# Optimization experiments

Hardware: AMD Instinct MI355X
Metric: run time of the kernel (lower is better)

Reference implementation:

```python
import jax, jax.numpy as jnp
import numpy as np

ROUNDS = 2
N_NODES = 50000
N_EDGES = 800000
NODE_DIM = 128
EDGE_DIM = 32
ACT_DIM = 128


def setup_inputs() -> dict:
    key = jax.random.key(0)
    ks = jax.random.split(key, 10)
    hv = jax.random.normal(ks[0], (N_NODES, NODE_DIM), dtype=jnp.float32)
    he = jax.random.normal(ks[1], (N_EDGES, EDGE_DIM), dtype=jnp.float32)
    src = jax.random.randint(ks[2], (N_EDGES,), 0, N_NODES, dtype=jnp.int32)
    dst = jax.random.randint(ks[3], (N_EDGES,), 0, N_NODES, dtype=jnp.int32)
    cat_dim = 2 * NODE_DIM + EDGE_DIM  # 288
    W_msg = jax.random.normal(ks[4], (ROUNDS, cat_dim, ACT_DIM), dtype=jnp.float32) * 0.05
    b_msg = jax.random.normal(ks[5], (ROUNDS, ACT_DIM), dtype=jnp.float32) * 0.05
    W_ih = jax.random.normal(ks[6], (ROUNDS, ACT_DIM, 3 * NODE_DIM), dtype=jnp.float32) * 0.05
    W_hh = jax.random.normal(ks[7], (ROUNDS, NODE_DIM, 3 * NODE_DIM), dtype=jnp.float32) * 0.05
    b_ih = jax.random.normal(ks[8], (ROUNDS, 3 * NODE_DIM), dtype=jnp.float32) * 0.05
    b_hh = jax.random.normal(ks[9], (ROUNDS, 3 * NODE_DIM), dtype=jnp.float32) * 0.05
    return {"hv": hv, "he": he, "src": src, "dst": dst,
            "W_msg": W_msg, "b_msg": b_msg,
            "W_ih": W_ih, "W_hh": W_hh, "b_ih": b_ih, "b_hh": b_hh}


def _gru_cell(x, h, W_ih, W_hh, b_ih, b_hh):
    # torch.nn.GRUCell math, gate order (r, z, n)
    gi = x @ W_ih + b_ih  # [N, 3H]
    gh = h @ W_hh + b_hh  # [N, 3H]
    ir, iz, in_ = jnp.split(gi, 3, axis=-1)
    hr, hz, hn = jnp.split(gh, 3, axis=-1)
    r = jax.nn.sigmoid(ir + hr)
    z = jax.nn.sigmoid(iz + hz)
    n = jnp.tanh(in_ + r * hn)
    return (1.0 - z) * n + z * h


def reference(hv, he, src, dst, W_msg, b_msg, W_ih, W_hh, b_ih, b_hh):
    N, nd = hv.shape
    for t in range(ROUNDS):
        # Linear on concat([hv_src, hv_dst, he]) == sum of block matmuls
        Ws = W_msg[t, :nd]          # src block
        Wd = W_msg[t, nd:2 * nd]    # dst block
        We = W_msg[t, 2 * nd:]      # edge block
        msg = hv[src] @ Ws + hv[dst] @ Wd + he @ We + b_msg[t]  # [E, act]
        a = jax.ops.segment_sum(msg, dst, num_segments=N)        # per-node sum over incoming edges
        hv = _gru_cell(a, hv, W_ih[t], W_hh[t], b_ih[t], b_hh[t])
    return hv
```

## Files before the change

kernel.cpp:

```cpp
#include <hip/hip_runtime.h>

#define N_NODES 50000
#define N_EDGES 800000
#define ND 128
#define ED 32
#define AD 128
#define CAT 288
#define G3 384

#define XPAD 296
#define KSTEPS 9
#define SCAN_BS 512

typedef unsigned short ushort_t;
typedef __attribute__((ext_vector_type(8))) short bfrag;
typedef __attribute__((ext_vector_type(4))) float f32x4;

__device__ __forceinline__ unsigned int f2bf(float f) {
    unsigned int u = __float_as_uint(f);
    return (u + 0x7FFFu + ((u >> 16) & 1u)) >> 16;
}
__device__ __forceinline__ void split2(float a, float b,
                                       unsigned int& hi, unsigned int& lo) {
    const unsigned int ha = f2bf(a), hb = f2bf(b);
    const float ra = a - __uint_as_float(ha << 16);
    const float rb = b - __uint_as_float(hb << 16);
    hi = ha | (hb << 16);
    lo = f2bf(ra) | (f2bf(rb) << 16);
}
__device__ __forceinline__ void split1(float a, ushort_t& hi, ushort_t& lo) {
    const unsigned int ha = f2bf(a);
    const float ra = a - __uint_as_float(ha << 16);
    hi = (ushort_t)ha;
    lo = (ushort_t)f2bf(ra);
}

__global__ __launch_bounds__(256) void hist_kernel(
    const int* __restrict__ dst, int* __restrict__ deg)
{
    const int e = blockIdx.x * 256 + threadIdx.x;
    if (e < N_EDGES) atomicAdd(&deg[dst[e]], 1);
}

__global__ __launch_bounds__(SCAN_BS) void scan_block_kernel(
    const int* __restrict__ in, int* __restrict__ out,
    int* __restrict__ bsum, int n)
{
    __shared__ int s[SCAN_BS];
    const int g = blockIdx.x * SCAN_BS + threadIdx.x;
    const int v = (g < n) ? in[g] : 0;
    s[threadIdx.x] = v;
    __syncthreads();
    for (int off = 1; off < SCAN_BS; off <<= 1) {
        const int x = (threadIdx.x >= off) ? s[threadIdx.x - off] : 0;
        __syncthreads();
        s[threadIdx.x] += x;
        __syncthreads();
    }
    if (g < n) out[g] = s[threadIdx.x] - v;
    if (threadIdx.x == SCAN_BS - 1) bsum[blockIdx.x] = s[threadIdx.x];
}

__global__ __launch_bounds__(128) void scan_sums_kernel(int* __restrict__ bsum, int nb)
{
    __shared__ int s[128];
    const int i = threadIdx.x;
    s[i] = (i < nb) ? bsum[i] : 0;
    __syncthreads();
    if (i == 0) {
        int acc = 0;
        for (int k = 0; k < nb; ++k) { const int t = s[k]; s[k] = acc; acc += t; }
    }
    __syncthreads();
    if (i < nb) bsum[i] = s[i];
}

__global__ __launch_bounds__(SCAN_BS) void scan_add_kernel(
    int* __restrict__ rowptr, int* __restrict__ cursor,
    const int* __restrict__ bsum, int n)
{
    const int g = blockIdx.x * SCAN_BS + threadIdx.x;
    if (g < n) {
        const int v = rowptr[g] + bsum[blockIdx.x];
        rowptr[g] = v;
        cursor[g] = v;
    }
}

__global__ __launch_bounds__(256) void fill_kernel(
    const int* __restrict__ dst, const int* __restrict__ src,
    int* __restrict__ cursor, int* __restrict__ perm,
    int* __restrict__ src_sorted)
{
    const int e = blockIdx.x * 256 + threadIdx.x;
    if (e < N_EDGES) {
        const int p = atomicAdd(&cursor[dst[e]], 1);
        perm[p] = e;
        src_sorted[p] = src[e];
    }
}

__global__ __launch_bounds__(256) void esum_kernel(
    const float* __restrict__ he, const int* __restrict__ perm,
    const int* __restrict__ rowptr, float* __restrict__ E)
{
    const int id = blockIdx.x * 256 + threadIdx.x;
    if (id >= N_NODES * ED) return;
    const int v = id >> 5, c = id & 31;
    const int r0 = rowptr[v], r1 = rowptr[v + 1];
    float s = 0.f;
    int i = r0;
    for (; i + 4 <= r1; i += 4) {
        const int p0 = perm[i],     p1 = perm[i + 1];
        const int p2 = perm[i + 2], p3 = perm[i + 3];
        const float a = he[(size_t)p0 * ED + c];
        const float b = he[(size_t)p1 * ED + c];
        const float d = he[(size_t)p2 * ED + c];
        const float f = he[(size_t)p3 * ED + c];
        s += (a + b) + (d + f);
    }
    for (; i < r1; ++i)
        s += he[(size_t)perm[i] * ED + c];
    E[(size_t)v * ED + c] = s;
}

__global__ __launch_bounds__(256) void convert_w_kernel(
    const float* __restrict__ W,
    ushort_t* __restrict__ Wt_hi, ushort_t* __restrict__ Wt_lo)
{
    const int id = blockIdx.x * 256 + threadIdx.x;
    if (id >= 2 * CAT * AD) return;
    const int n = id & (AD - 1);
    const int k = (id >> 7) % CAT;
    const int t = id / (CAT * AD);
    const float w = W[(size_t)t * CAT * AD + (size_t)k * AD + n];
    const unsigned int hi = f2bf(w);
    const float r = w - __uint_as_float(hi << 16);
    const size_t o = (size_t)t * AD * CAT + (size_t)n * CAT + k;
    Wt_hi[o] = (ushort_t)hi;
    Wt_lo[o] = (ushort_t)f2bf(r);
}

__global__ __launch_bounds__(256) void convert_gatew_kernel(
    const float* __restrict__ W_ih, const float* __restrict__ W_hh,
    ushort_t* __restrict__ Bih_hi, ushort_t* __restrict__ Bih_lo,
    ushort_t* __restrict__ Bhh_hi, ushort_t* __restrict__ Bhh_lo)
{
    const int id = blockIdx.x * 256 + threadIdx.x;
    if (id >= 196608) return;
    const int t   = id / 98304;
    const int rem = id % 98304;
    const int mat = rem / 49152;
    const int q   = rem % 49152;
    const int nt = q / 2048,  r1 = q % 2048;
    const int ks = r1 / 512,  r2 = r1 % 512;
    const int kq = r2 / 128,  r3 = r2 % 128;
    const int lr = r3 / 8,    j  = r3 % 8;
    const int n = nt * 16 + lr;
    const int k = ks * 32 + kq * 8 + j;
    const float* W = mat ? W_hh : W_ih;
    const float w = W[(size_t)t * ND * G3 + (size_t)k * G3 + n];
    const unsigned int hi = f2bf(w);
    const float res = w - __uint_as_float(hi << 16);
    const size_t o = (size_t)t * 49152 + q;
    if (mat) { Bhh_hi[o] = (ushort_t)hi; Bhh_lo[o] = (ushort_t)f2bf(res); }
    else     { Bih_hi[o] = (ushort_t)hi; Bih_lo[o] = (ushort_t)f2bf(res); }
}

__global__ __launch_bounds__(256) void agg_kernel(
    const float* __restrict__ hv, const int* __restrict__ src_sorted,
    const int* __restrict__ rowptr,
    ushort_t* __restrict__ S_hi, ushort_t* __restrict__ S_lo)
{
    const int v = blockIdx.x * 4 + (threadIdx.x >> 6);
    if (v >= N_NODES) return;
    const int lane = threadIdx.x & 63;
    const int r0 = rowptr[v], r1 = rowptr[v + 1];
    const float2* hv2 = (const float2*)hv;
    float sx = 0.f, sy = 0.f;
    int i = r0;
    for (; i + 8 <= r1; i += 8) {
        const int s0 = src_sorted[i],     s1 = src_sorted[i + 1];
        const int s2 = src_sorted[i + 2], s3 = src_sorted[i + 3];
        const int s4 = src_sorted[i + 4], s5 = src_sorted[i + 5];
        const int s6 = src_sorted[i + 6], s7 = src_sorted[i + 7];
        const float2 a = hv2[(size_t)s0 * 64 + lane];
        const float2 b = hv2[(size_t)s1 * 64 + lane];
        const float2 c = hv2[(size_t)s2 * 64 + lane];
        const float2 d = hv2[(size_t)s3 * 64 + lane];
        const float2 e = hv2[(size_t)s4 * 64 + lane];
        const float2 f = hv2[(size_t)s5 * 64 + lane];
        const float2 g = hv2[(size_t)s6 * 64 + lane];
        const float2 h = hv2[(size_t)s7 * 64 + lane];
        sx += ((a.x + b.x) + (c.x + d.x)) + ((e.x + f.x) + (g.x + h.x));
        sy += ((a.y + b.y) + (c.y + d.y)) + ((e.y + f.y) + (g.y + h.y));
    }
    for (; i < r1; ++i) {
        const float2 a = hv2[(size_t)src_sorted[i] * 64 + lane];
        sx += a.x; sy += a.y;
    }
    unsigned int h, l;
    split2(sx, sy, h, l);
    ((unsigned int*)S_hi)[(size_t)v * 64 + lane] = h;
    ((unsigned int*)S_lo)[(size_t)v * 64 + lane] = l;
}

__global__ __launch_bounds__(256, 2) void fused_msg_gru_kernel(
    const ushort_t* __restrict__ S_hi, const ushort_t* __restrict__ S_lo,
    const float* __restrict__ h_cur, const float* __restrict__ E,
    const int* __restrict__ rowptr,
    const ushort_t* __restrict__ Wt_hi, const ushort_t* __restrict__ Wt_lo,
    const float* __restrict__ bmsg,
    const ushort_t* __restrict__ Bih_hi, const ushort_t* __restrict__ Bih_lo,
    const ushort_t* __restrict__ Bhh_hi, const ushort_t* __restrict__ Bhh_lo,
    const float* __restrict__ b_ih, const float* __restrict__ b_hh,
    float* __restrict__ h_out)
{
    __shared__ __align__(16) char smem[67072];
    ushort_t* xh    = (ushort_t*)smem;
    ushort_t* xl    = xh + 32 * XPAD;
    ushort_t* sh_hi = xl + 32 * XPAD;
    ushort_t* sh_lo = sh_hi + 32 * 136;
    ushort_t* sa_hi = (ushort_t*)smem;
    ushort_t* sa_lo = sa_hi + 32 * 136;
    float* grz = (float*)smem;
    float* gin = grz + 32 * 260;
    float* ghn = gin + 32 * 132;
    __shared__ float sdeg[32];

    const int t    = threadIdx.x;
    const int wave = t >> 6;
    const int lane = t & 63;
    const int kq   = lane >> 4;
    const int lr   = lane & 15;
    const int n0   = blockIdx.x * 32;

    bfrag mbh[2][KSTEPS], mbl[2][KSTEPS];
    float mbias[2];
    #pragma unroll
    for (int nt = 0; nt < 2; ++nt) {
        const int n = wave * 32 + nt * 16 + lr;
        mbias[nt] = bmsg[n];
        const ushort_t* ph = Wt_hi + (size_t)n * CAT + kq * 8;
        const ushort_t* pl = Wt_lo + (size_t)n * CAT + kq * 8;
        #pragma unroll
        for (int ks = 0; ks < KSTEPS; ++ks) {
            mbh[nt][ks] = *(const bfrag*)(ph + ks * 32);
            mbl[nt][ks] = *(const bfrag*)(pl + ks * 32);
        }
    }

    {
        const int row = t >> 3, c8 = t & 7;
        const int n = min(n0 + row, N_NODES - 1);
        if (t < 32) {
            const int nn = min(n0 + t, N_NODES - 1);
            sdeg[t] = (float)(rowptr[nn + 1] - rowptr[nn]);
        }
        {
            const uint4* ph = (const uint4*)(S_hi + (size_t)n * ND + c8 * 16);
            const uint4* pl = (const uint4*)(S_lo + (size_t)n * ND + c8 * 16);
            *(uint4*)&xh[row * XPAD + c8 * 16]     = ph[0];
            *(uint4*)&xh[row * XPAD + c8 * 16 + 8] = ph[1];
            *(uint4*)&xl[row * XPAD + c8 * 16]     = pl[0];
            *(uint4*)&xl[row * XPAD + c8 * 16 + 8] = pl[1];
        }
        {
            const float degf = (float)(rowptr[n + 1] - rowptr[n]);
            const float4* hp = (const float4*)(h_cur + (size_t)n * ND + c8 * 16);
            const float4 v0 = hp[0], v1 = hp[1], v2 = hp[2], v3 = hp[3];
            uint4 h0, h1, l0, l1;
            split2(v0.x, v0.y, h0.x, l0.x); split2(v0.z, v0.w, h0.y, l0.y);
            split2(v1.x, v1.y, h0.z, l0.z); split2(v1.z, v1.w, h0.w, l0.w);
            split2(v2.x, v2.y, h1.x, l1.x); split2(v2.z, v2.w, h1.y, l1.y);
            split2(v3.x, v3.y, h1.z, l1.z); split2(v3.z, v3.w, h1.w, l1.w);
            const int so = row * 136 + c8 * 16;
            *(uint4*)(sh_hi + so) = h0;  *(uint4*)(sh_hi + so + 8) = h1;
            *(uint4*)(sh_lo + so) = l0;  *(uint4*)(sh_lo + so + 8) = l1;
            uint4 g0, g1, m0, m1;
            split2(v0.x * degf, v0.y * degf, g0.x, m0.x); split2(v0.z * degf, v0.w * degf, g0.y, m0.y);
            split2(v1.x * degf, v1.y * degf, g0.z, m0.z); split2(v1.z * degf, v1.w * degf, g0.w, m0.w);
            split2(v2.x * degf, v2.y * degf, g1.x, m1.x); split2(v2.z * degf, v2.w * degf, g1.y, m1.y);
            split2(v3.x * degf, v3.y * degf, g1.z, m1.z); split2(v3.z * degf, v3.w * degf, g1.w, m1.w);
            *(uint4*)&xh[row * XPAD + ND + c8 * 16]     = g0;
            *(uint4*)&xh[row * XPAD + ND + c8 * 16 + 8] = g1;
            *(uint4*)&xl[row * XPAD + ND + c8 * 16]     = m0;
            *(uint4*)&xl[row * XPAD + ND + c8 * 16 + 8] = m1;
        }
        {
            const float4 e4 = *(const float4*)(E + (size_t)n * ED + c8 * 4);
            uint2 h0, l0;
            split2(e4.x, e4.y, h0.x, l0.x); split2(e4.z, e4.w, h0.y, l0.y);
            *(uint2*)&xh[row * XPAD + 2 * ND + c8 * 4] = h0;
            *(uint2*)&xl[row * XPAD + 2 * ND + c8 * 4] = l0;
        }
    }
    __syncthreads();

    f32x4 acc00 = {0.f,0.f,0.f,0.f}, acc01 = {0.f,0.f,0.f,0.f};
    f32x4 acc10 = {0.f,0.f,0.f,0.f}, acc11 = {0.f,0.f,0.f,0.f};
    #pragma unroll
    for (int ks = 0; ks < KSTEPS; ++ks) {
        const int ko = ks * 32 + kq * 8;
        const bfrag a0h = *(const bfrag*)&xh[lr * XPAD + ko];
        const bfrag a0l = *(const bfrag*)&xl[lr * XPAD + ko];
        const bfrag a1h = *(const bfrag*)&xh[(16 + lr) * XPAD + ko];
        const bfrag a1l = *(const bfrag*)&xl[(16 + lr) * XPAD + ko];
        acc00 = __builtin_amdgcn_mfma_f32_16x16x32_bf16(a0h, mbh[0][ks], acc00, 0, 0, 0);
        acc00 = __builtin_amdgcn_mfma_f32_16x16x32_bf16(a0l, mbh[0][ks], acc00, 0, 0, 0);
        acc00 = __builtin_amdgcn_mfma_f32_16x16x32_bf16(a0h, mbl[0][ks], acc00, 0, 0, 0);
        acc01 = __builtin_amdgcn_mfma_f32_16x16x32_bf16(a0h, mbh[1][ks], acc01, 0, 0, 0);
        acc01 = __builtin_amdgcn_mfma_f32_16x16x32_bf16(a0l, mbh[1][ks], acc01, 0, 0, 0);
        acc01 = __builtin_amdgcn_mfma_f32_16x16x32_bf16(a0h, mbl[1][ks], acc01, 0, 0, 0);
        acc10 = __builtin_amdgcn_mfma_f32_16x16x32_bf16(a1h, mbh[0][ks], acc10, 0, 0, 0);
        acc10 = __builtin_amdgcn_mfma_f32_16x16x32_bf16(a1l, mbh[0][ks], acc10, 0, 0, 0);
        acc10 = __builtin_amdgcn_mfma_f32_16x16x32_bf16(a1h, mbl[0][ks], acc10, 0, 0, 0);
        acc11 = __builtin_amdgcn_mfma_f32_16x16x32_bf16(a1h, mbh[1][ks], acc11, 0, 0, 0);
        acc11 = __builtin_amdgcn_mfma_f32_16x16x32_bf16(a1l, mbh[1][ks], acc11, 0, 0, 0);
        acc11 = __builtin_amdgcn_mfma_f32_16x16x32_bf16(a1h, mbl[1][ks], acc11, 0, 0, 0);
    }
    __syncthreads();

    #pragma unroll
    for (int r = 0; r < 4; ++r) {
        const int row0 = kq * 4 + r;
        const int row1 = 16 + kq * 4 + r;
        const int c0 = wave * 32 + lr, c1 = wave * 32 + 16 + lr;
        ushort_t h, l;
        split1(acc00[r] + sdeg[row0] * mbias[0], h, l);
        sa_hi[row0 * 136 + c0] = h; sa_lo[row0 * 136 + c0] = l;
        split1(acc01[r] + sdeg[row0] * mbias[1], h, l);
        sa_hi[row0 * 136 + c1] = h; sa_lo[row0 * 136 + c1] = l;
        split1(acc10[r] + sdeg[row1] * mbias[0], h, l);
        sa_hi[row1 * 136 + c0] = h; sa_lo[row1 * 136 + c0] = l;
        split1(acc11[r] + sdeg[row1] * mbias[1], h, l);
        sa_hi[row1 * 136 + c1] = h; sa_lo[row1 * 136 + c1] = l;
    }
    __syncthreads();

    f32x4 acc_i[2][6], acc_h[2][6];
    #pragma unroll
    for (int m = 0; m < 2; ++m)
        #pragma unroll
        for (int nt = 0; nt < 6; ++nt) {
            acc_i[m][nt] = (f32x4){0.f, 0.f, 0.f, 0.f};
            acc_h[m][nt] = (f32x4){0.f, 0.f, 0.f, 0.f};
        }

    #pragma unroll
    for (int ks = 0; ks < 4; ++ks) {
        bfrag afh[2], afl[2], hfh[2], hfl[2];
        #pragma unroll
        for (int m = 0; m < 2; ++m) {
            const int ao = (m * 16 + lr) * 136 + ks * 32 + kq * 8;
            afh[m] = *(const bfrag*)(sa_hi + ao);
            afl[m] = *(const bfrag*)(sa_lo + ao);
            hfh[m] = *(const bfrag*)(sh_hi + ao);
            hfl[m] = *(const bfrag*)(sh_lo + ao);
        }
        #pragma unroll
        for (int nt = 0; nt < 6; ++nt) {
            const int gnt = wave * 6 + nt;
            const int bo = (((gnt * 4 + ks) * 4 + kq) * 16 + lr) * 8;
            const bfrag bih_h = *(const bfrag*)(Bih_hi + bo);
            const bfrag bih_l = *(const bfrag*)(Bih_lo + bo);
            const bfrag bhh_h = *(const bfrag*)(Bhh_hi + bo);
            const bfrag bhh_l = *(const bfrag*)(Bhh_lo + bo);
            #pragma unroll
            for (int m = 0; m < 2; ++m) {
                acc_i[m][nt] = __builtin_amdgcn_mfma_f32_16x16x32_bf16(afh[m], bih_h, acc_i[m][nt], 0, 0, 0);
                acc_i[m][nt] = __builtin_amdgcn_mfma_f32_16x16x32_bf16(afl[m], bih_h, acc_i[m][nt], 0, 0, 0);
                acc_i[m][nt] = __builtin_amdgcn_mfma_f32_16x16x32_bf16(afh[m], bih_l, acc_i[m][nt], 0, 0, 0);
                acc_h[m][nt] = __builtin_amdgcn_mfma_f32_16x16x32_bf16(hfh[m], bhh_h, acc_h[m][nt], 0, 0, 0);
                acc_h[m][nt] = __builtin_amdgcn_mfma_f32_16x16x32_bf16(hfl[m], bhh_h, acc_h[m][nt], 0, 0, 0);
                acc_h[m][nt] = __builtin_amdgcn_mfma_f32_16x16x32_bf16(hfh[m], bhh_l, acc_h[m][nt], 0, 0, 0);
            }
        }
    }
    __syncthreads();

    #pragma unroll
    for (int nt = 0; nt < 6; ++nt) {
        const int gcol = wave * 96 + nt * 16 + lr;
        if (gcol < 256) {
            const float bias = b_ih[gcol] + b_hh[gcol];
            #pragma unroll
            for (int m = 0; m < 2; ++m)
                #pragma unroll
                for (int r = 0; r < 4; ++r)
                    grz[(m * 16 + kq * 4 + r) * 260 + gcol] =
                        acc_i[m][nt][r] + acc_h[m][nt][r] + bias;
        } else {
            const int cc = gcol - 256;
            const float bi = b_ih[gcol], bh2 = b_hh[gcol];
            #pragma unroll
            for (int m = 0; m < 2; ++m)
                #pragma unroll
                for (int r = 0; r < 4; ++r) {
                    const int rw = m * 16 + kq * 4 + r;
                    gin[rw * 132 + cc] = acc_i[m][nt][r] + bi;
                    ghn[rw * 132 + cc] = acc_h[m][nt][r] + bh2;
                }
        }
    }
    __syncthreads();

    for (int idx = t; idx < 32 * ND; idx += 256) {
        const int nl = idx >> 7, cc = idx & 127;
        const int n = n0 + nl;
        if (n < N_NODES) {
            const float rp  = grz[nl * 260 + cc];
            const float zp  = grz[nl * 260 + 128 + cc];
            const float inp = gin[nl * 132 + cc];
            const float hnp = ghn[nl * 132 + cc];
            const float r = 1.f / (1.f + expf(-rp));
            const float z = 1.f / (1.f + expf(-zp));
            const float nn = tanhf(inp + r * hnp);
            h_out[(size_t)n * ND + cc] =
                (1.f - z) * nn + z * h_cur[(size_t)n * ND + cc];
        }
    }
}

extern "C" void kernel_launch(void* const* d_in, const int* in_sizes, int n_in,
                              void* d_out, int out_size, void* d_ws, size_t ws_size,
                              hipStream_t stream)
{
    const float* hv   = (const float*)d_in[0];
    const float* he   = (const float*)d_in[1];
    const int*   src  = (const int*)d_in[2];
    const int*   dst  = (const int*)d_in[3];
    const float* Wmsg = (const float*)d_in[4];
    const float* bmsg = (const float*)d_in[5];
    const float* Wih  = (const float*)d_in[6];
    const float* Whh  = (const float*)d_in[7];
    const float* bih  = (const float*)d_in[8];
    const float* bhh  = (const float*)d_in[9];
    float* out = (float*)d_out;

    const int nscan = ((N_NODES + SCAN_BS - 1) / SCAN_BS) * SCAN_BS;
    const int nblk  = nscan / SCAN_BS;

    char* p = (char*)d_ws;
    ushort_t* S_hi = (ushort_t*)p;            p += (size_t)N_NODES * ND * 2;
    ushort_t* S_lo = (ushort_t*)p;            p += (size_t)N_NODES * ND * 2;
    float* E = (float*)p;                     p += (size_t)N_NODES * ED * 4;
    ushort_t* Wt_hi = (ushort_t*)p;           p += (size_t)2 * AD * CAT * 2;
    ushort_t* Wt_lo = (ushort_t*)p;           p += (size_t)2 * AD * CAT * 2;
    ushort_t* Bih_hi = (ushort_t*)p;          p += (size_t)2 * G3 * ND * 2;
    ushort_t* Bih_lo = (ushort_t*)p;          p += (size_t)2 * G3 * ND * 2;
    ushort_t* Bhh_hi = (ushort_t*)p;          p += (size_t)2 * G3 * ND * 2;
    ushort_t* Bhh_lo = (ushort_t*)p;          p += (size_t)2 * G3 * ND * 2;
    int* deg    = (int*)p;                    p += (size_t)nscan * 4;
    int* rowptr = (int*)p;                    p += (size_t)nscan * 4;
    int* cursor = (int*)p;                    p += (size_t)nscan * 4;
    int* bsum   = (int*)p;                    p += 128 * 4;
    int* perm   = (int*)p;                    p += (size_t)N_EDGES * 4;
    int* src_sorted = (int*)p;                p += (size_t)N_EDGES * 4;

    convert_w_kernel<<<(2 * CAT * AD + 255) / 256, 256, 0, stream>>>(Wmsg, Wt_hi, Wt_lo);
    convert_gatew_kernel<<<768, 256, 0, stream>>>(Wih, Whh, Bih_hi, Bih_lo, Bhh_hi, Bhh_lo);

    hipMemsetAsync(deg, 0, (size_t)nscan * 4, stream);
    hist_kernel<<<(N_EDGES + 255) / 256, 256, 0, stream>>>(dst, deg);
    scan_block_kernel<<<nblk, SCAN_BS, 0, stream>>>(deg, rowptr, bsum, nscan);
    scan_sums_kernel<<<1, 128, 0, stream>>>(bsum, nblk);
    scan_add_kernel<<<nblk, SCAN_BS, 0, stream>>>(rowptr, cursor, bsum, nscan);
    fill_kernel<<<(N_EDGES + 255) / 256, 256, 0, stream>>>(dst, src, cursor, perm, src_sorted);
    esum_kernel<<<(N_NODES * ED + 255) / 256, 256, 0, stream>>>(he, perm, rowptr, E);

    const int tile_blocks = (N_NODES + 31) / 32;

    for (int t = 0; t < 2; ++t) {
        const float* h_cur = (t == 0) ? hv : out;
        agg_kernel<<<(N_NODES + 3) / 4, 256, 0, stream>>>(
            h_cur, src_sorted, rowptr, S_hi, S_lo);
        fused_msg_gru_kernel<<<tile_blocks, 256, 0, stream>>>(
            S_hi, S_lo, h_cur, E, rowptr,
            Wt_hi + (size_t)t * AD * CAT, Wt_lo + (size_t)t * AD * CAT,
            bmsg + (size_t)t * AD,
            Bih_hi + (size_t)t * G3 * ND, Bih_lo + (size_t)t * G3 * ND,
            Bhh_hi + (size_t)t * G3 * ND, Bhh_lo + (size_t)t * G3 * ND,
            bih + (size_t)t * G3, bhh + (size_t)t * G3, out);
    }
}
```

Baseline: 583.4 us.

## Reuse h tile for dst-message term, stream weights, fuse GRU epilogue in registers

The degree-scaled h copy in the message GEMM's K dimension is dropped. The kernel now reuses the existing swizzled h tile, computing the dst term as a separate accumulator that is multiplied by degree afterwards. Message weights are streamed from global memory in MFMA fragment order instead of being held in registers. Gate weights are permuted so each wave owns matching r/z/n columns, which lets the GRU nonlinearity run directly on accumulators with fast exp instead of going through shared-memory staging. Shared memory and register use shrink so three blocks can fit per CU, at the cost of more global weight loads and fast-math approximations of sigmoid and tanh.

```diff
diff --git a/kernel.cpp b/kernel.cpp
--- a/kernel.cpp
+++ b/kernel.cpp
@@ -8,8 +8,7 @@
 #define CAT 288
 #define G3 384
 
-#define XPAD 296
-#define KSTEPS 9
+#define XP2 168
 #define SCAN_BS 512
 
 typedef unsigned short ushort_t;
@@ -130,13 +129,20 @@
 {
     const int id = blockIdx.x * 256 + threadIdx.x;
     if (id >= 2 * CAT * AD) return;
-    const int n = id & (AD - 1);
-    const int k = (id >> 7) % CAT;
-    const int t = id / (CAT * AD);
-    const float w = W[(size_t)t * CAT * AD + (size_t)k * AD + n];
+    const int tt = id / (CAT * AD);
+    const int q  = id % (CAT * AD);
+    const int j  = q & 7;
+    const int lr = (q >> 3) & 15;
+    const int kq = (q >> 7) & 3;
+    const int ks = (q >> 9) % 9;
+    const int gnt = q / 4608;
+    const int n  = gnt * 16 + lr;
+    const int kn = ks * 32 + kq * 8 + j;
+    const int ko = kn < 128 ? kn : (kn < 160 ? kn + 128 : kn - 32);
+    const float w = W[(size_t)tt * CAT * AD + (size_t)ko * AD + n];
     const unsigned int hi = f2bf(w);
     const float r = w - __uint_as_float(hi << 16);
-    const size_t o = (size_t)t * AD * CAT + (size_t)n * CAT + k;
+    const size_t o = (size_t)tt * (CAT * AD) + q;
     Wt_hi[o] = (ushort_t)hi;
     Wt_lo[o] = (ushort_t)f2bf(r);
 }
@@ -156,7 +162,9 @@
     const int ks = r1 / 512,  r2 = r1 % 512;
     const int kq = r2 / 128,  r3 = r2 % 128;
     const int lr = r3 / 8,    j  = r3 % 8;
-    const int n = nt * 16 + lr;
+    const int wv = nt / 6, within = nt % 6;
+    const int gate = within % 3, hf = within / 3;
+    const int n = gate * 128 + wv * 32 + hf * 16 + lr;
     const int k = ks * 32 + kq * 8 + j;
     const float* W = mat ? W_hh : W_ih;
     const float w = W[(size_t)t * ND * G3 + (size_t)k * G3 + n];
@@ -205,7 +213,7 @@
     ((unsigned int*)S_lo)[(size_t)v * 64 + lane] = l;
 }
 
-__global__ __launch_bounds__(256, 2) void fused_msg_gru_kernel(
+__global__ __launch_bounds__(256, 3) void fused_msg_gru_kernel(
     const ushort_t* __restrict__ S_hi, const ushort_t* __restrict__ S_lo,
     const float* __restrict__ h_cur, const float* __restrict__ E,
     const int* __restrict__ rowptr,
@@ -216,16 +224,13 @@
     const float* __restrict__ b_ih, const float* __restrict__ b_hh,
     float* __restrict__ h_out)
 {
-    __shared__ __align__(16) char smem[67072];
+    __shared__ __align__(16) char smem[37888];
     ushort_t* xh    = (ushort_t*)smem;
-    ushort_t* xl    = xh + 32 * XPAD;
-    ushort_t* sh_hi = xl + 32 * XPAD;
-    ushort_t* sh_lo = sh_hi + 32 * 136;
+    ushort_t* xl    = xh + 32 * XP2;
+    ushort_t* sh_hi = xl + 32 * XP2;
+    ushort_t* sh_lo = sh_hi + 32 * 128;
     ushort_t* sa_hi = (ushort_t*)smem;
-    ushort_t* sa_lo = sa_hi + 32 * 136;
-    float* grz = (float*)smem;
-    float* gin = grz + 32 * 260;
-    float* ghn = gin + 32 * 132;
+    ushort_t* sa_lo = sa_hi + 32 * 128;
     __shared__ float sdeg[32];
 
     const int t    = threadIdx.x;
@@ -235,20 +240,8 @@
     const int lr   = lane & 15;
     const int n0   = blockIdx.x * 32;
 
-    bfrag mbh[2][KSTEPS], mbl[2][KSTEPS];
-    float mbias[2];
-    #pragma unroll
-    for (int nt = 0; nt < 2; ++nt) {
-        const int n = wave * 32 + nt * 16 + lr;
-        mbias[nt] = bmsg[n];
-        const ushort_t* ph = Wt_hi + (size_t)n * CAT + kq * 8;
-        const ushort_t* pl = Wt_lo + (size_t)n * CAT + kq * 8;
-        #pragma unroll
-        for (int ks = 0; ks < KSTEPS; ++ks) {
-            mbh[nt][ks] = *(const bfrag*)(ph + ks * 32);
-            mbl[nt][ks] = *(const bfrag*)(pl + ks * 32);
-        }
-    }
+    const float mbias0 = bmsg[wave * 32 + lr];
+    const float mbias1 = bmsg[wave * 32 + 16 + lr];
 
     {
         const int row = t >> 3, c8 = t & 7;
@@ -260,13 +253,12 @@
         {
             const uint4* ph = (const uint4*)(S_hi + (size_t)n * ND + c8 * 16);
             const uint4* pl = (const uint4*)(S_lo + (size_t)n * ND + c8 * 16);
-            *(uint4*)&xh[row * XPAD + c8 * 16]     = ph[0];
-            *(uint4*)&xh[row * XPAD + c8 * 16 + 8] = ph[1];
-            *(uint4*)&xl[row * XPAD + c8 * 16]     = pl[0];
-            *(uint4*)&xl[row * XPAD + c8 * 16 + 8] = pl[1];
+            *(uint4*)&xh[row * XP2 + c8 * 16]     = ph[0];
+            *(uint4*)&xh[row * XP2 + c8 * 16 + 8] = ph[1];
+            *(uint4*)&xl[row * XP2 + c8 * 16]     = pl[0];
+            *(uint4*)&xl[row * XP2 + c8 * 16 + 8] = pl[1];
         }
         {
-            const float degf = (float)(rowptr[n + 1] - rowptr[n]);
             const float4* hp = (const float4*)(h_cur + (size_t)n * ND + c8 * 16);
             const float4 v0 = hp[0], v1 = hp[1], v2 = hp[2], v3 = hp[3];
             uint4 h0, h1, l0, l1;
@@ -274,151 +266,160 @@
             split2(v1.x, v1.y, h0.z, l0.z); split2(v1.z, v1.w, h0.w, l0.w);
             split2(v2.x, v2.y, h1.x, l1.x); split2(v2.z, v2.w, h1.y, l1.y);
             split2(v3.x, v3.y, h1.z, l1.z); split2(v3.z, v3.w, h1.w, l1.w);
-            const int so = row * 136 + c8 * 16;
-            *(uint4*)(sh_hi + so) = h0;  *(uint4*)(sh_hi + so + 8) = h1;
-            *(uint4*)(sh_lo + so) = l0;  *(uint4*)(sh_lo + so + 8) = l1;
-            uint4 g0, g1, m0, m1;
-            split2(v0.x * degf, v0.y * degf, g0.x, m0.x); split2(v0.z * degf, v0.w * degf, g0.y, m0.y);
-            split2(v1.x * degf, v1.y * degf, g0.z, m0.z); split2(v1.z * degf, v1.w * degf, g0.w, m0.w);
-            split2(v2.x * degf, v2.y * degf, g1.x, m1.x); split2(v2.z * degf, v2.w * degf, g1.y, m1.y);
-            split2(v3.x * degf, v3.y * degf, g1.z, m1.z); split2(v3.z * degf, v3.w * degf, g1.w, m1.w);
-            *(uint4*)&xh[row * XPAD + ND + c8 * 16]     = g0;
-            *(uint4*)&xh[row * XPAD + ND + c8 * 16 + 8] = g1;
-            *(uint4*)&xl[row * XPAD + ND + c8 * 16]     = m0;
-            *(uint4*)&xl[row * XPAD + ND + c8 * 16 + 8] = m1;
+            const int so  = (row * 128 + c8 * 16)     ^ ((row & 7) << 3);
+            const int so2 = (row * 128 + c8 * 16 + 8) ^ ((row & 7) << 3);
+            *(uint4*)(sh_hi + so)  = h0;  *(uint4*)(sh_hi + so2) = h1;
+            *(uint4*)(sh_lo + so)  = l0;  *(uint4*)(sh_lo + so2) = l1;
         }
         {
             const float4 e4 = *(const float4*)(E + (size_t)n * ED + c8 * 4);
             uint2 h0, l0;
             split2(e4.x, e4.y, h0.x, l0.x); split2(e4.z, e4.w, h0.y, l0.y);
-            *(uint2*)&xh[row * XPAD + 2 * ND + c8 * 4] = h0;
-            *(uint2*)&xl[row * XPAD + 2 * ND + c8 * 4] = l0;
-        }
-    }
-    __syncthreads();
-
-    f32x4 acc00 = {0.f,0.f,0.f,0.f}, acc01 = {0.f,0.f,0.f,0.f};
-    f32x4 acc10 = {0.f,0.f,0.f,0.f}, acc11 = {0.f,0.f,0.f,0.f};
-    #pragma unroll
-    for (int ks = 0; ks < KSTEPS; ++ks) {
-        const int ko = ks * 32 + kq * 8;
-        const bfrag a0h = *(const bfrag*)&xh[lr * XPAD + ko];
-        const bfrag a0l = *(const bfrag*)&xl[lr * XPAD + ko];
-        const bfrag a1h = *(const bfrag*)&xh[(16 + lr) * XPAD + ko];
-        const bfrag a1l = *(const bfrag*)&xl[(16 + lr) * XPAD + ko];
-        acc00 = __builtin_amdgcn_mfma_f32_16x16x32_bf16(a0h, mbh[0][ks], acc00, 0, 0, 0);
-        acc00 = __builtin_amdgcn_mfma_f32_16x16x32_bf16(a0l, mbh[0][ks], acc00, 0, 0, 0);
-        acc00 = __builtin_amdgcn_mfma_f32_16x16x32_bf16(a0h, mbl[0][ks], acc00, 0, 0, 0);
-        acc01 = __builtin_amdgcn_mfma_f32_16x16x32_bf16(a0h, mbh[1][ks], acc01, 0, 0, 0);
-        acc01 = __builtin_amdgcn_mfma_f32_16x16x32_bf16(a0l, mbh[1][ks], acc01, 0, 0, 0);
-        acc01 = __builtin_amdgcn_mfma_f32_16x16x32_bf16(a0h, mbl[1][ks], acc01, 0, 0, 0);
-        acc10 = __builtin_amdgcn_mfma_f32_16x16x32_bf16(a1h, mbh[0][ks], acc10, 0, 0, 0);
-        acc10 = __builtin_amdgcn_mfma_f32_16x16x32_bf16(a1l, mbh[0][ks], acc10, 0, 0, 0);
-        acc10 = __builtin_amdgcn_mfma_f32_16x16x32_bf16(a1h, mbl[0][ks], acc10, 0, 0, 0);
-        acc11 = __builtin_amdgcn_mfma_f32_16x16x32_bf16(a1h, mbh[1][ks], acc11, 0, 0, 0);
-        acc11 = __builtin_amdgcn_mfma_f32_16x16x32_bf16(a1l, mbh[1][ks], acc11, 0, 0, 0);
-        acc11 = __builtin_amdgcn_mfma_f32_16x16x32_bf16(a1h, mbl[1][ks], acc11, 0, 0, 0);
+            *(uint2*)&xh[row * XP2 + 128 + c8 * 4] = h0;
+            *(uint2*)&xl[row * XP2 + 128 + c8 * 4] = l0;
+        }
+    }
+    __syncthreads();
+
+    f32x4 aX00 = {0.f,0.f,0.f,0.f}, aX01 = {0.f,0.f,0.f,0.f};
+    f32x4 aX10 = {0.f,0.f,0.f,0.f}, aX11 = {0.f,0.f,0.f,0.f};
+    f32x4 aP00 = {0.f,0.f,0.f,0.f}, aP01 = {0.f,0.f,0.f,0.f};
+    f32x4 aP10 = {0.f,0.f,0.f,0.f}, aP11 = {0.f,0.f,0.f,0.f};
+    {
+        const size_t wb0 = (size_t)(wave * 2 + 0) * 4608 + kq * 128 + lr * 8;
+        const size_t wb1 = (size_t)(wave * 2 + 1) * 4608 + kq * 128 + lr * 8;
+        const ushort_t* wh0 = Wt_hi + wb0;  const ushort_t* wl0 = Wt_lo + wb0;
+        const ushort_t* wh1 = Wt_hi + wb1;  const ushort_t* wl1 = Wt_lo + wb1;
+        #pragma unroll
+        for (int ks = 0; ks < 5; ++ks) {
+            const int ko = ks * 32 + kq * 8;
+            const bfrag a0h = *(const bfrag*)&xh[lr * XP2 + ko];
+            const bfrag a0l = *(const bfrag*)&xl[lr * XP2 + ko];
+            const bfrag a1h = *(const bfrag*)&xh[(16 + lr) * XP2 + ko];
+            const bfrag a1l = *(const bfrag*)&xl[(16 + lr) * XP2 + ko];
+            const bfrag b0h = *(const bfrag*)(wh0 + ks * 512);
+            const bfrag b0l = *(const bfrag*)(wl0 + ks * 512);
+            const bfrag b1h = *(const bfrag*)(wh1 + ks * 512);
+            const bfrag b1l = *(const bfrag*)(wl1 + ks * 512);
+            aX00 = __builtin_amdgcn_mfma_f32_16x16x32_bf16(a0h, b0h, aX00, 0, 0, 0);
+            aX00 = __builtin_amdgcn_mfma_f32_16x16x32_bf16(a0l, b0h, aX00, 0, 0, 0);
+            aX00 = __builtin_amdgcn_mfma_f32_16x16x32_bf16(a0h, b0l, aX00, 0, 0, 0);
+            aX01 = __builtin_amdgcn_mfma_f32_16x16x32_bf16(a0h, b1h, aX01, 0, 0, 0);
+            aX01 = __builtin_amdgcn_mfma_f32_16x16x32_bf16(a0l, b1h, aX01, 0, 0, 0);
+            aX01 = __builtin_amdgcn_mfma_f32_16x16x32_bf16(a0h, b1l, aX01, 0, 0, 0);
+            aX10 = __builtin_amdgcn_mfma_f32_16x16x32_bf16(a1h, b0h, aX10, 0, 0, 0);
+            aX10 = __builtin_amdgcn_mfma_f32_16x16x32_bf16(a1l, b0h, aX10, 0, 0, 0);
+            aX10 = __builtin_amdgcn_mfma_f32_16x16x32_bf16(a1h, b0l, aX10, 0, 0, 0);
+            aX11 = __builtin_amdgcn_mfma_f32_16x16x32_bf16(a1h, b1h, aX11, 0, 0, 0);
+            aX11 = __builtin_amdgcn_mfma_f32_16x16x32_bf16(a1l, b1h, aX11, 0, 0, 0);
+            aX11 = __builtin_amdgcn_mfma_f32_16x16x32_bf16(a1h, b1l, aX11, 0, 0, 0);
+        }
+        #pragma unroll
+        for (int ks = 5; ks < 9; ++ks) {
+            const int hk = (ks - 5) * 32 + kq * 8;
+            const int o0 = (lr * 128 + hk)        ^ ((lr & 7) << 3);
+            const int o1 = ((16 + lr) * 128 + hk) ^ ((lr & 7) << 3);
+            const bfrag a0h = *(const bfrag*)(sh_hi + o0);
+            const bfrag a0l = *(const bfrag*)(sh_lo + o0);
+            const bfrag a1h = *(const bfrag*)(sh_hi + o1);
+            const bfrag a1l = *(const bfrag*)(sh_lo + o1);
+            const bfrag b0h = *(const bfrag*)(wh0 + ks * 512);
+            const bfrag b0l = *(const bfrag*)(wl0 + ks * 512);
+            const bfrag b1h = *(const bfrag*)(wh1 + ks * 512);
+            const bfrag b1l = *(const bfrag*)(wl1 + ks * 512);
+            aP00 = __builtin_amdgcn_mfma_f32_16x16x32_bf16(a0h, b0h, aP00, 0, 0, 0);
+            aP00 = __builtin_amdgcn_mfma_f32_16x16x32_bf16(a0l, b0h, aP00, 0, 0, 0);
+            aP00 = __builtin_amdgcn_mfma_f32_16x16x32_bf16(a0h, b0l, aP00, 0, 0, 0);
+            aP01 = __builtin_amdgcn_mfma_f32_16x16x32_bf16(a0h, b1h, aP01, 0, 0, 0);
+            aP01 = __builtin_amdgcn_mfma_f32_16x16x32_bf16(a0l, b1h, aP01, 0, 0, 0);
+            aP01 = __builtin_amdgcn_mfma_f32_16x16x32_bf16(a0h, b1l, aP01, 0, 0, 0);
+            aP10 = __builtin_amdgcn_mfma_f32_16x16x32_bf16(a1h, b0h, aP10, 0, 0, 0);
+            aP10 = __builtin_amdgcn_mfma_f32_16x16x32_bf16(a1l, b0h, aP10, 0, 0, 0);
+            aP10 = __builtin_amdgcn_mfma_f32_16x16x32_bf16(a1h, b0l, aP10, 0, 0, 0);
+            aP11 = __builtin_amdgcn_mfma_f32_16x16x32_bf16(a1h, b1h, aP11, 0, 0, 0);
+            aP11 = __builtin_amdgcn_mfma_f32_16x16x32_bf16(a1l, b1h, aP11, 0, 0, 0);
+            aP11 = __builtin_amdgcn_mfma_f32_16x16x32_bf16(a1h, b1l, aP11, 0, 0, 0);
+        }
     }
     __syncthreads();
 
     #pragma unroll
     for (int r = 0; r < 4; ++r) {
         const int row0 = kq * 4 + r;
-        const int row1 = 16 + kq * 4 + r;
-        const int c0 = wave * 32 + lr, c1 = wave * 32 + 16 + lr;
+        const int row1 = 16 + row0;
+        const int c0 = wave * 32 + lr, c1 = c0 + 16;
+        const float d0 = sdeg[row0], d1 = sdeg[row1];
         ushort_t h, l;
-        split1(acc00[r] + sdeg[row0] * mbias[0], h, l);
-        sa_hi[row0 * 136 + c0] = h; sa_lo[row0 * 136 + c0] = l;
-        split1(acc01[r] + sdeg[row0] * mbias[1], h, l);
-        sa_hi[row0 * 136 + c1] = h; sa_lo[row0 * 136 + c1] = l;
-        split1(acc10[r] + sdeg[row1] * mbias[0], h, l);
-        sa_hi[row1 * 136 + c0] = h; sa_lo[row1 * 136 + c0] = l;
-        split1(acc11[r] + sdeg[row1] * mbias[1], h, l);
-        sa_hi[row1 * 136 + c1] = h; sa_lo[row1 * 136 + c1] = l;
-    }
-    __syncthreads();
-
-    f32x4 acc_i[2][6], acc_h[2][6];
+        split1(aX00[r] + d0 * (aP00[r] + mbias0), h, l);
+        { const int o = (row0 * 128 + c0) ^ ((row0 & 7) << 3); sa_hi[o] = h; sa_lo[o] = l; }
+        split1(aX01[r] + d0 * (aP01[r] + mbias1), h, l);
+        { const int o = (row0 * 128 + c1) ^ ((row0 & 7) << 3); sa_hi[o] = h; sa_lo[o] = l; }
+        split1(aX10[r] + d1 * (aP10[r] + mbias0), h, l);
+        { const int o = (row1 * 128 + c0) ^ ((row1 & 7) << 3); sa_hi[o] = h; sa_lo[o] = l; }
+        split1(aX11[r] + d1 * (aP11[r] + mbias1), h, l);
+        { const int o = (row1 * 128 + c1) ^ ((row1 & 7) << 3); sa_hi[o] = h; sa_lo[o] = l; }
+    }
+    __syncthreads();
+
     #pragma unroll
-    for (int m = 0; m < 2; ++m)
+    for (int half = 0; half < 2; ++half) {
+        f32x4 ai[2][3], ah2[2][3];
         #pragma unroll
-        for (int nt = 0; nt < 6; ++nt) {
-            acc_i[m][nt] = (f32x4){0.f, 0.f, 0.f, 0.f};
-            acc_h[m][nt] = (f32x4){0.f, 0.f, 0.f, 0.f};
-        }
-
-    #pragma unroll
-    for (int ks = 0; ks < 4; ++ks) {
-        bfrag afh[2], afl[2], hfh[2], hfl[2];
+        for (int m = 0; m < 2; ++m)
+            #pragma unroll
+            for (int g = 0; g < 3; ++g) {
+                ai[m][g]  = (f32x4){0.f, 0.f, 0.f, 0.f};
+                ah2[m][g] = (f32x4){0.f, 0.f, 0.f, 0.f};
+            }
         #pragma unroll
-        for (int m = 0; m < 2; ++m) {
-            const int ao = (m * 16 + lr) * 136 + ks * 32 + kq * 8;
-            afh[m] = *(const bfrag*)(sa_hi + ao);
-            afl[m] = *(const bfrag*)(sa_lo + ao);
-            hfh[m] = *(const bfrag*)(sh_hi + ao);
-            hfl[m] = *(const bfrag*)(sh_lo + ao);
-        }
-        #pragma unroll
-        for (int nt = 0; nt < 6; ++nt) {
-            const int gnt = wave * 6 + nt;
-            const int bo = (((gnt * 4 + ks) * 4 + kq) * 16 + lr) * 8;
-            const bfrag bih_h = *(const bfrag*)(Bih_hi + bo);
-            const bfrag bih_l = *(const bfrag*)(Bih_lo + bo);
-            const bfrag bhh_h = *(const bfrag*)(Bhh_hi + bo);
-            const bfrag bhh_l = *(const bfrag*)(Bhh_lo + bo);
+        for (int ks = 0; ks < 4; ++ks) {
+            bfrag afh[2], afl[2], hfh[2], hfl[2];
             #pragma unroll
             for (int m = 0; m < 2; ++m) {
-                acc_i[m][nt] = __builtin_amdgcn_mfma_f32_16x16x32_bf16(afh[m], bih_h, acc_i[m][nt], 0, 0, 0);
-                acc_i[m][nt] = __builtin_amdgcn_mfma_f32_16x16x32_bf16(afl[m], bih_h, acc_i[m][nt], 0, 0, 0);
-                acc_i[m][nt] = __builtin_amdgcn_mfma_f32_16x16x32_bf16(afh[m], bih_l, acc_i[m][nt], 0, 0, 0);
-                acc_h[m][nt] = __builtin_amdgcn_mfma_f32_16x16x32_bf16(hfh[m], bhh_h, acc_h[m][nt], 0, 0, 0);
-                acc_h[m][nt] = __builtin_amdgcn_mfma_f32_16x16x32_bf16(hfl[m], bhh_h, acc_h[m][nt], 0, 0, 0);
-                acc_h[m][nt] = __builtin_amdgcn_mfma_f32_16x16x32_bf16(hfh[m], bhh_l, acc_h[m][nt], 0, 0, 0);
+                const int o = ((m * 16 + lr) * 128 + ks * 32 + kq * 8) ^ ((lr & 7) << 3);
+                afh[m] = *(const bfrag*)(sa_hi + o);
+                afl[m] = *(const bfrag*)(sa_lo + o);
+                hfh[m] = *(const bfrag*)(sh_hi + o);
+                hfl[m] = *(const bfrag*)(sh_lo + o);
             }
-        }
-    }
-    __syncthreads();
-
-    #pragma unroll
-    for (int nt = 0; nt < 6; ++nt) {
-        const int gcol = wave * 96 + nt * 16 + lr;
-        if (gcol < 256) {
-            const float bias = b_ih[gcol] + b_hh[gcol];
             #pragma unroll
-            for (int m = 0; m < 2; ++m)
+            for (int g = 0; g < 3; ++g) {
+                const int gnt = wave * 6 + half * 3 + g;
+                const size_t bo = (size_t)(gnt * 2048 + ks * 512 + kq * 128 + lr * 8);
+                const bfrag bih_h = *(const bfrag*)(Bih_hi + bo);
+                const bfrag bih_l = *(const bfrag*)(Bih_lo + bo);
+                const bfrag bhh_h = *(const bfrag*)(Bhh_hi + bo);
+                const bfrag bhh_l = *(const bfrag*)(Bhh_lo + bo);
                 #pragma unroll
-                for (int r = 0; r < 4; ++r)
-                    grz[(m * 16 + kq * 4 + r) * 260 + gcol] =
-                        acc_i[m][nt][r] + acc_h[m][nt][r] + bias;
-        } else {
-            const int cc = gcol - 256;
-            const float bi = b_ih[gcol], bh2 = b_hh[gcol];
+                for (int m = 0; m < 2; ++m) {
+                    ai[m][g]  = __builtin_amdgcn_mfma_f32_16x16x32_bf16(afh[m], bih_h, ai[m][g], 0, 0, 0);
+                    ai[m][g]  = __builtin_amdgcn_mfma_f32_16x16x32_bf16(afl[m], bih_h, ai[m][g], 0, 0, 0);
+                    ai[m][g]  = __builtin_amdgcn_mfma_f32_16x16x32_bf16(afh[m], bih_l, ai[m][g], 0, 0, 0);
+                    ah2[m][g] = __builtin_amdgcn_mfma_f32_16x16x32_bf16(hfh[m], bhh_h, ah2[m][g], 0, 0, 0);
+                    ah2[m][g] = __builtin_amdgcn_mfma_f32_16x16x32_bf16(hfl[m], bhh_h, ah2[m][g], 0, 0, 0);
+                    ah2[m][g] = __builtin_amdgcn_mfma_f32_16x16x32_bf16(hfh[m], bhh_l, ah2[m][g], 0, 0, 0);
+                }
+            }
+        }
+        const int c = wave * 32 + half * 16 + lr;
+        const float br  = b_ih[c] + b_hh[c];
+        const float bz  = b_ih[128 + c] + b_hh[128 + c];
+        const float bin = b_ih[256 + c];
+        const float bhn = b_hh[256 + c];
+        #pragma unroll
+        for (int m = 0; m < 2; ++m)
             #pragma unroll
-            for (int m = 0; m < 2; ++m)
-                #pragma unroll
-                for (int r = 0; r < 4; ++r) {
-                    const int rw = m * 16 + kq * 4 + r;
-                    gin[rw * 132 + cc] = acc_i[m][nt][r] + bi;
-                    ghn[rw * 132 + cc] = acc_h[m][nt][r] + bh2;
+            for (int r = 0; r < 4; ++r) {
+                const int nn = n0 + m * 16 + kq * 4 + r;
+                if (nn < N_NODES) {
+                    const float hc = h_cur[(size_t)nn * ND + c];
+                    const float rg = 1.f / (1.f + __expf(-(ai[m][0][r] + ah2[m][0][r] + br)));
+                    const float zg = 1.f / (1.f + __expf(-(ai[m][1][r] + ah2[m][1][r] + bz)));
+                    const float npre = ai[m][2][r] + bin + rg * (ah2[m][2][r] + bhn);
+                    const float ng = 1.f - 2.f / (__expf(2.f * npre) + 1.f);
+                    h_out[(size_t)nn * ND + c] = (1.f - zg) * ng + zg * hc;
                 }
-        }
-    }
-    __syncthreads();
-
-    for (int idx = t; idx < 32 * ND; idx += 256) {
-        const int nl = idx >> 7, cc = idx & 127;
-        const int n = n0 + nl;
-        if (n < N_NODES) {
-            const float rp  = grz[nl * 260 + cc];
-            const float zp  = grz[nl * 260 + 128 + cc];
-            const float inp = gin[nl * 132 + cc];
-            const float hnp = ghn[nl * 132 + cc];
-            const float r = 1.f / (1.f + expf(-rp));
-            const float z = 1.f / (1.f + expf(-zp));
-            const float nn = tanhf(inp + r * hnp);
-            h_out[(size_t)n * ND + cc] =
-                (1.f - z) * nn + z * h_cur[(size_t)n * ND + cc];
-        }
+            }
     }
 }
 
```

Result: faster. 528.8 us (-9.4%).
